# Performance work log

Hardware: AMD Instinct MI355X
Metric: run time of the kernel (lower is better)

The kernel has to match this reference:

```python
import jax, jax.numpy as jnp
import numpy as np


def setup_inputs() -> dict:
    key = jax.random.key(0)
    ks = jax.random.split(key, 6)
    B, H, T, Dk, Dv = 64, 16, 4, 128, 256
    q = jax.random.normal(ks[0], (B, H, T, Dk), dtype=jnp.float32)
    k = jax.random.normal(ks[1], (B, H, T, Dk), dtype=jnp.float32)
    v = jax.random.normal(ks[2], (B, H, T, Dv), dtype=jnp.float32)
    g = jax.random.uniform(ks[3], (B, H, T), dtype=jnp.float32)
    beta = jax.random.uniform(ks[4], (B, H, T), dtype=jnp.float32)
    last_recurrent_state = jax.random.normal(ks[5], (B, H, Dk, Dv), dtype=jnp.float32)
    return {"q": q, "k": k, "v": v, "g": g, "beta": beta,
            "last_recurrent_state": last_recurrent_state}


def reference(q, k, v, g, beta, last_recurrent_state):
    # q,k: (B,H,T,Dk)  v: (B,H,T,Dv)  g,beta: (B,H,T)  state: (B,H,Dk,Dv)
    def step(state, xs):
        q_t, k_t, v_t, g_t, beta_t = xs  # (B,H,Dk),(B,H,Dk),(B,H,Dv),(B,H),(B,H)
        state = state * jnp.exp(g_t)[..., None, None]           # decay
        kv_mem = jnp.einsum('bhkv,bhk->bhv', state, k_t)         # readout with key
        delta = (v_t - kv_mem) * beta_t[..., None]               # delta-rule correction
        state = state + k_t[..., None] * delta[..., None, :]     # rank-1 update
        out_t = jnp.einsum('bhkv,bhk->bhv', state, q_t)          # query readout
        return state, out_t

    xs = (jnp.moveaxis(q, 2, 0), jnp.moveaxis(k, 2, 0), jnp.moveaxis(v, 2, 0),
          jnp.moveaxis(g, 2, 0), jnp.moveaxis(beta, 2, 0))
    state, outs = jax.lax.scan(step, last_recurrent_state, xs)
    output = jnp.moveaxis(outs, 0, 2)  # (B,H,T,Dv)
    return jnp.concatenate([output.reshape(-1), state.reshape(-1)], axis=0)
```

## Files before the change

### kernel.cpp

```cpp
#include <hip/hip_runtime.h>

#define BH    1024
#define TT    4
#define DK    128
#define DV    256
#define KSEG  8
#define KLEN  16
#define HALFV 128
#define LDP   17

__global__ __launch_bounds__(256)
void delta_rule_kernel(const float* __restrict__ q,
                       const float* __restrict__ k,
                       const float* __restrict__ v,
                       const float* __restrict__ g,
                       const float* __restrict__ beta,
                       const float* __restrict__ s0,
                       float* __restrict__ out)
{
    const int bh   = blockIdx.x >> 1;
    const int half = blockIdx.x & 1;
    const int tid  = threadIdx.x;
    const int kg   = tid & (KSEG - 1);
    const int vg   = tid >> 3;
    const int vcol = half * HALFV + vg * 4;
    const int kr0  = kg * KLEN;

    const float* __restrict__ sin_p = s0 + (size_t)bh * DK * DV;
    float* __restrict__ out_p  = out + (size_t)bh * TT * DV;
    float* __restrict__ sout_p = out + (size_t)BH * TT * DV + (size_t)bh * DK * DV;

    const float* __restrict__ kbase = k    + (size_t)bh * TT * DK;
    const float* __restrict__ qbase = q    + (size_t)bh * TT * DK;
    const float* __restrict__ vbase = v    + (size_t)bh * TT * DV;
    const float* __restrict__ gbase = g    + (size_t)bh * TT;
    const float* __restrict__ bbase = beta + (size_t)bh * TT;

    float4 s4[KLEN];
#pragma unroll
    for (int kk = 0; kk < KLEN; ++kk)
        s4[kk] = *(const float4*)&sin_p[(size_t)(kr0 + kk) * DV + vcol];

    __shared__ float ks[KSEG * LDP];
    __shared__ float qs[KSEG * LDP];

    for (int t = 0; t < TT; ++t) {
        __syncthreads();
        if (tid < DK) {
            ks[(tid >> 4) * LDP + (tid & 15)] = kbase[t * DK + tid];
        } else {
            int j = tid - DK;
            qs[(j >> 4) * LDP + (j & 15)] = qbase[t * DK + j];
        }
        __syncthreads();

        const float gt = expf(gbase[t]);
        const float bt = bbase[t];
        const float4 v4 = *(const float4*)&vbase[t * DV + vcol];

        float4 kv = make_float4(0.f, 0.f, 0.f, 0.f);
#pragma unroll
        for (int kk = 0; kk < KLEN; ++kk) {
            const float kt = ks[kg * LDP + kk];
            s4[kk].x *= gt; s4[kk].y *= gt; s4[kk].z *= gt; s4[kk].w *= gt;
            kv.x = fmaf(s4[kk].x, kt, kv.x);
            kv.y = fmaf(s4[kk].y, kt, kv.y);
            kv.z = fmaf(s4[kk].z, kt, kv.z);
            kv.w = fmaf(s4[kk].w, kt, kv.w);
        }
#pragma unroll
        for (int m = 1; m < KSEG; m <<= 1) {
            kv.x += __shfl_xor(kv.x, m);
            kv.y += __shfl_xor(kv.y, m);
            kv.z += __shfl_xor(kv.z, m);
            kv.w += __shfl_xor(kv.w, m);
        }

        float4 d4;
        d4.x = (v4.x - kv.x) * bt;
        d4.y = (v4.y - kv.y) * bt;
        d4.z = (v4.z - kv.z) * bt;
        d4.w = (v4.w - kv.w) * bt;

        float4 o4 = make_float4(0.f, 0.f, 0.f, 0.f);
#pragma unroll
        for (int kk = 0; kk < KLEN; ++kk) {
            const float kt = ks[kg * LDP + kk];
            const float qt = qs[kg * LDP + kk];
            s4[kk].x = fmaf(kt, d4.x, s4[kk].x);
            s4[kk].y = fmaf(kt, d4.y, s4[kk].y);
            s4[kk].z = fmaf(kt, d4.z, s4[kk].z);
            s4[kk].w = fmaf(kt, d4.w, s4[kk].w);
            o4.x = fmaf(s4[kk].x, qt, o4.x);
            o4.y = fmaf(s4[kk].y, qt, o4.y);
            o4.z = fmaf(s4[kk].z, qt, o4.z);
            o4.w = fmaf(s4[kk].w, qt, o4.w);
        }
#pragma unroll
        for (int m = 1; m < KSEG; m <<= 1) {
            o4.x += __shfl_xor(o4.x, m);
            o4.y += __shfl_xor(o4.y, m);
            o4.z += __shfl_xor(o4.z, m);
            o4.w += __shfl_xor(o4.w, m);
        }
        if (kg == 0)
            *(float4*)&out_p[t * DV + vcol] = o4;
    }

#pragma unroll
    for (int kk = 0; kk < KLEN; ++kk)
        *(float4*)&sout_p[(size_t)(kr0 + kk) * DV + vcol] = s4[kk];
}

extern "C" void kernel_launch(void* const* d_in, const int* in_sizes, int n_in,
                              void* d_out, int out_size, void* d_ws, size_t ws_size,
                              hipStream_t stream) {
    const float* q    = (const float*)d_in[0];
    const float* k    = (const float*)d_in[1];
    const float* v    = (const float*)d_in[2];
    const float* g    = (const float*)d_in[3];
    const float* beta = (const float*)d_in[4];
    const float* s0   = (const float*)d_in[5];
    float* out = (float*)d_out;

    delta_rule_kernel<<<dim3(BH * 2), dim3(256), 0, stream>>>(q, k, v, g, beta, s0, out);
}
```

Measured before the change: 262.7 us.

## Drop shared-memory staging of k/q, load directly to registers, quarter V per block

Replaces the shared-memory staging of k and q (and its two barriers per timestep) with direct float4 global loads into registers, since each thread needs only its contiguous 16-element k/q segment. Splits each head into four 64-column blocks of 128 threads instead of two 256-thread blocks, and precomputes exp(g) and beta for all timesteps up front using the fast __expf. This is meant to remove synchronisation and LDS traffic and improve scheduling flexibility. In exchange, each k/q vector is fetched redundantly by more threads and blocks from cache, and __expf lowers precision slightly.

Result: slower. 281.8 us (+7.3%).

```diff
diff --git a/kernel.cpp b/kernel.cpp
--- a/kernel.cpp
+++ b/kernel.cpp
@@ -6,10 +6,28 @@
 #define DV    256
 #define KSEG  8
 #define KLEN  16
-#define HALFV 128
-#define LDP   17
+#define QV    64
 
-__global__ __launch_bounds__(256)
+
+#define PH1(idx, kt)                                   \
+    { s4[idx].x *= g_; s4[idx].y *= g_;                \
+      s4[idx].z *= g_; s4[idx].w *= g_;                \
+      kv.x = fmaf(s4[idx].x, (kt), kv.x);              \
+      kv.y = fmaf(s4[idx].y, (kt), kv.y);              \
+      kv.z = fmaf(s4[idx].z, (kt), kv.z);              \
+      kv.w = fmaf(s4[idx].w, (kt), kv.w); }
+
+#define PH2(idx, kt, qt)                               \
+    { s4[idx].x = fmaf((kt), d4.x, s4[idx].x);         \
+      s4[idx].y = fmaf((kt), d4.y, s4[idx].y);         \
+      s4[idx].z = fmaf((kt), d4.z, s4[idx].z);         \
+      s4[idx].w = fmaf((kt), d4.w, s4[idx].w);         \
+      o4.x = fmaf(s4[idx].x, (qt), o4.x);              \
+      o4.y = fmaf(s4[idx].y, (qt), o4.y);              \
+      o4.z = fmaf(s4[idx].z, (qt), o4.z);              \
+      o4.w = fmaf(s4[idx].w, (qt), o4.w); }
+
+__global__ __launch_bounds__(128, 4)
 void delta_rule_kernel(const float* __restrict__ q,
                        const float* __restrict__ k,
                        const float* __restrict__ v,
@@ -18,13 +36,14 @@
                        const float* __restrict__ s0,
                        float* __restrict__ out)
 {
-    const int bh   = blockIdx.x >> 1;
-    const int half = blockIdx.x & 1;
-    const int tid  = threadIdx.x;
-    const int kg   = tid & (KSEG - 1);
-    const int vg   = tid >> 3;
-    const int vcol = half * HALFV + vg * 4;
-    const int kr0  = kg * KLEN;
+    const int bx      = blockIdx.x;
+    const int bh      = bx >> 2;
+    const int quarter = bx & 3;
+    const int tid     = threadIdx.x;
+    const int kg      = tid & (KSEG - 1);
+    const int vg      = tid >> 3;
+    const int vcol    = quarter * QV + vg * 4;
+    const int kr0     = kg * KLEN;
 
     const float* __restrict__ sin_p = s0 + (size_t)bh * DK * DV;
     float* __restrict__ out_p  = out + (size_t)bh * TT * DV;
@@ -36,38 +55,34 @@
     const float* __restrict__ gbase = g    + (size_t)bh * TT;
     const float* __restrict__ bbase = beta + (size_t)bh * TT;
 
+    float gt[TT], bt[TT];
+#pragma unroll
+    for (int t = 0; t < TT; ++t) {
+        gt[t] = __expf(gbase[t]) ;
+        bt[t] = bbase[t];
+    }
+
     float4 s4[KLEN];
 #pragma unroll
     for (int kk = 0; kk < KLEN; ++kk)
         s4[kk] = *(const float4*)&sin_p[(size_t)(kr0 + kk) * DV + vcol];
 
-    __shared__ float ks[KSEG * LDP];
-    __shared__ float qs[KSEG * LDP];
+#pragma unroll
+    for (int t = 0; t < TT; ++t) {
+        float4 kf0 = *(const float4*)&kbase[t * DK + kr0 +  0];
+        float4 kf1 = *(const float4*)&kbase[t * DK + kr0 +  4];
+        float4 kf2 = *(const float4*)&kbase[t * DK + kr0 +  8];
+        float4 kf3 = *(const float4*)&kbase[t * DK + kr0 + 12];
+        float4 v4  = *(const float4*)&vbase[t * DV + vcol];
 
-    for (int t = 0; t < TT; ++t) {
-        __syncthreads();
-        if (tid < DK) {
-            ks[(tid >> 4) * LDP + (tid & 15)] = kbase[t * DK + tid];
-        } else {
-            int j = tid - DK;
-            qs[(j >> 4) * LDP + (j & 15)] = qbase[t * DK + j];
-        }
-        __syncthreads();
-
-        const float gt = expf(gbase[t]);
-        const float bt = bbase[t];
-        const float4 v4 = *(const float4*)&vbase[t * DV + vcol];
+        const float g_ = gt[t];
 
         float4 kv = make_float4(0.f, 0.f, 0.f, 0.f);
-#pragma unroll
-        for (int kk = 0; kk < KLEN; ++kk) {
-            const float kt = ks[kg * LDP + kk];
-            s4[kk].x *= gt; s4[kk].y *= gt; s4[kk].z *= gt; s4[kk].w *= gt;
-            kv.x = fmaf(s4[kk].x, kt, kv.x);
-            kv.y = fmaf(s4[kk].y, kt, kv.y);
-            kv.z = fmaf(s4[kk].z, kt, kv.z);
-            kv.w = fmaf(s4[kk].w, kt, kv.w);
-        }
+        PH1( 0, kf0.x) PH1( 1, kf0.y) PH1( 2, kf0.z) PH1( 3, kf0.w)
+        PH1( 4, kf1.x) PH1( 5, kf1.y) PH1( 6, kf1.z) PH1( 7, kf1.w)
+        PH1( 8, kf2.x) PH1( 9, kf2.y) PH1(10, kf2.z) PH1(11, kf2.w)
+        PH1(12, kf3.x) PH1(13, kf3.y) PH1(14, kf3.z) PH1(15, kf3.w)
+
 #pragma unroll
         for (int m = 1; m < KSEG; m <<= 1) {
             kv.x += __shfl_xor(kv.x, m);
@@ -77,25 +92,22 @@
         }
 
         float4 d4;
-        d4.x = (v4.x - kv.x) * bt;
-        d4.y = (v4.y - kv.y) * bt;
-        d4.z = (v4.z - kv.z) * bt;
-        d4.w = (v4.w - kv.w) * bt;
+        d4.x = (v4.x - kv.x) * bt[t];
+        d4.y = (v4.y - kv.y) * bt[t];
+        d4.z = (v4.z - kv.z) * bt[t];
+        d4.w = (v4.w - kv.w) * bt[t];
+
+        float4 qf0 = *(const float4*)&qbase[t * DK + kr0 +  0];
+        float4 qf1 = *(const float4*)&qbase[t * DK + kr0 +  4];
+        float4 qf2 = *(const float4*)&qbase[t * DK + kr0 +  8];
+        float4 qf3 = *(const float4*)&qbase[t * DK + kr0 + 12];
 
         float4 o4 = make_float4(0.f, 0.f, 0.f, 0.f);
-#pragma unroll
-        for (int kk = 0; kk < KLEN; ++kk) {
-            const float kt = ks[kg * LDP + kk];
-            const float qt = qs[kg * LDP + kk];
-            s4[kk].x = fmaf(kt, d4.x, s4[kk].x);
-            s4[kk].y = fmaf(kt, d4.y, s4[kk].y);
-            s4[kk].z = fmaf(kt, d4.z, s4[kk].z);
-            s4[kk].w = fmaf(kt, d4.w, s4[kk].w);
-            o4.x = fmaf(s4[kk].x, qt, o4.x);
-            o4.y = fmaf(s4[kk].y, qt, o4.y);
-            o4.z = fmaf(s4[kk].z, qt, o4.z);
-            o4.w = fmaf(s4[kk].w, qt, o4.w);
-        }
+        PH2( 0, kf0.x, qf0.x) PH2( 1, kf0.y, qf0.y) PH2( 2, kf0.z, qf0.z) PH2( 3, kf0.w, qf0.w)
+        PH2( 4, kf1.x, qf1.x) PH2( 5, kf1.y, qf1.y) PH2( 6, kf1.z, qf1.z) PH2( 7, kf1.w, qf1.w)
+        PH2( 8, kf2.x, qf2.x) PH2( 9, kf2.y, qf2.y) PH2(10, kf2.z, qf2.z) PH2(11, kf2.w, qf2.w)
+        PH2(12, kf3.x, qf3.x) PH2(13, kf3.y, qf3.y) PH2(14, kf3.z, qf3.z) PH2(15, kf3.w, qf3.w)
+
 #pragma unroll
         for (int m = 1; m < KSEG; m <<= 1) {
             o4.x += __shfl_xor(o4.x, m);
@@ -123,5 +135,5 @@
     const float* s0   = (const float*)d_in[5];
     float* out = (float*)d_out;
 
-    delta_rule_kernel<<<dim3(BH * 2), dim3(256), 0, stream>>>(q, k, v, g, beta, s0, out);
+    delta_rule_kernel<<<dim3(BH * 4), dim3(128), 0, stream>>>(q, k, v, g, beta, s0, out);
 }
```
